# Performance work log

Hardware: AMD Instinct MI355X
Metric: run time of the kernel (lower is better)

Reference implementation:

```python
import jax, jax.numpy as jnp
import numpy as np

N_NODES = 100000
N_EDGES = 800000
R = 3
NEG_SLOPE = 0.2


def gat_conv(x, src, dst, W, al, ar, b, n_nodes):
    """One DGL-style GATConv for a single relation.
    x: [N, F_in], W: [F_in, H, D], al/ar/b: [H, D]. Returns [N, H, D]."""
    h = jnp.einsum('nf,fhd->nhd', x, W)          # [N, H, D]
    el = (h * al).sum(-1)                         # [N, H]
    er = (h * ar).sum(-1)                         # [N, H]
    e = jax.nn.leaky_relu(el[src] + er[dst], NEG_SLOPE)   # [E, H]
    # segment softmax over destination nodes
    m = jax.ops.segment_max(e, dst, num_segments=n_nodes)  # [N, H]
    ex = jnp.exp(e - m[dst])                                # [E, H]
    denom = jax.ops.segment_sum(ex, dst, num_segments=n_nodes)  # [N, H]
    alpha = ex / denom[dst]                                 # [E, H]
    msg = alpha[:, :, None] * h[src]                        # [E, H, D]
    out = jax.ops.segment_sum(msg, dst, num_segments=n_nodes)   # [N, H, D]
    return out + b


def setup_inputs() -> dict:
    key = jax.random.key(0)
    ks = jax.random.split(key, 12)
    d = {
        'x': jax.random.normal(ks[0], (N_NODES, 128), dtype=jnp.float32),
        'src': jax.random.randint(ks[1], (R, N_EDGES), 0, N_NODES, dtype=jnp.int32),
        'dst': jax.random.randint(ks[2], (R, N_EDGES), 0, N_NODES, dtype=jnp.int32),
        'W1': jax.random.normal(ks[3], (R, 128, 2, 64), dtype=jnp.float32) * 0.1,
        'al1': jax.random.normal(ks[4], (R, 2, 64), dtype=jnp.float32) * 0.1,
        'ar1': jax.random.normal(ks[5], (R, 2, 64), dtype=jnp.float32) * 0.1,
        'b1': jax.random.normal(ks[6], (R, 2, 64), dtype=jnp.float32) * 0.1,
        'W2': jax.random.normal(ks[7], (R, 128, 2, 64), dtype=jnp.float32) * 0.1,
        'al2': jax.random.normal(ks[8], (R, 2, 64), dtype=jnp.float32) * 0.1,
        'ar2': jax.random.normal(ks[9], (R, 2, 64), dtype=jnp.float32) * 0.1,
        'b2': jax.random.normal(ks[10], (R, 2, 64), dtype=jnp.float32) * 0.1,
    }
    return d


def reference(x, src, dst, W1, al1, ar1, b1, W2, al2, ar2, b2):
    n = x.shape[0]
    # layer 1: sum over relations (HeteroGraphConv aggregate='sum')
    h1 = sum(gat_conv(x, src[r], dst[r], W1[r], al1[r], ar1[r], b1[r], n)
             for r in range(R))                   # [N, 2, 64]
    h1 = jax.nn.relu(h1).reshape(n, -1)           # flatten heads -> [N, 128]
    # layer 2
    h2 = sum(gat_conv(h1, src[r], dst[r], W2[r], al2[r], ar2[r], b2[r], n)
             for r in range(R))                   # [N, 2, 64]
    return h2.mean(axis=1)                        # [N, 64]
```

## Files before the change

kernel.cpp:

```cpp
#include <hip/hip_runtime.h>
#include <hip/hip_bf16.h>
#include <math.h>

#define NF 128
#define NBKT 256
#define BCAP 11264
#define SPANCAP 2048

typedef __attribute__((ext_vector_type(8))) short short8v;
typedef __attribute__((ext_vector_type(4))) float float4v;

__device__ inline float leaky02(float v) { return v >= 0.0f ? v : 0.2f * v; }

__device__ inline unsigned short f2bf(float x) {
    unsigned u = __float_as_uint(x);
    u = u + 0x7fffu + ((u >> 16) & 1u);
    return (unsigned short)(u >> 16);
}
__device__ inline float bf2f(unsigned short h) {
    return __uint_as_float(((unsigned)h) << 16);
}

__device__ inline int rl_i(int v, int lane) {
    return __builtin_amdgcn_readlane(v, lane);
}
__device__ inline float rl_f(float v, int lane) {
    return __uint_as_float(__builtin_amdgcn_readlane(__float_as_uint(v), lane));
}

__global__ __launch_bounds__(256) void prep(
    const float* __restrict__ W1, const float* __restrict__ W2,
    const float* __restrict__ al1, const float* __restrict__ ar1,
    const float* __restrict__ b1,
    const float* __restrict__ al2, const float* __restrict__ ar2,
    const float* __restrict__ b2,
    unsigned short* __restrict__ WThi, unsigned short* __restrict__ WTlo,
    float* __restrict__ P, float* __restrict__ bs)
{
    int i = blockIdx.x * 256 + threadIdx.x;
    if (i < 6 * 16384) {
        int m = i >> 14, rem = i & 16383, k = rem >> 7, col = rem & 127;
        const float* Wm = (m < 3) ? W1 + (size_t)m * 16384
                                  : W2 + (size_t)(m - 3) * 16384;
        float v = Wm[k * 128 + col];
        unsigned short h = f2bf(v);
        WThi[(size_t)m * 16384 + col * 128 + k] = h;
        WTlo[(size_t)m * 16384 + col * 128 + k] = f2bf(v - bf2f(h));
    } else if (i < 6 * 16384 + 3072) {
        int idx = i - 6 * 16384;
        int m = idx >> 9, rem = idx & 511, f = rem >> 2, c = rem & 3;
        int head = c & 1;
        const float* Wm = (m < 3) ? W1 + (size_t)m * 16384
                                  : W2 + (size_t)(m - 3) * 16384;
        const float* vec;
        if (m < 3) vec = ((c < 2) ? al1 : ar1) + m * 128 + head * 64;
        else       vec = ((c < 2) ? al2 : ar2) + (m - 3) * 128 + head * 64;
        float s = 0.f;
        for (int d = 0; d < 64; d++) s += Wm[f * 128 + head * 64 + d] * vec[d];
        P[m * 512 + f * 4 + c] = s;
    } else if (i < 6 * 16384 + 3072 + 256) {
        int idx = i - 6 * 16384 - 3072;
        int layer = idx >> 7, cc = idx & 127;
        const float* b = layer ? b2 : b1;
        bs[layer * 128 + cc] = b[cc] + b[128 + cc] + b[256 + cc];
    }
}

__global__ __launch_bounds__(256) void bucket_count(
    const int* __restrict__ dst, int* __restrict__ bcnt,
    int E, int N, int span)
{
    __shared__ int h[NBKT];
    h[threadIdx.x] = 0;
    __syncthreads();
    const int tot = 3 * E;
    for (int e = blockIdx.x * 256 + threadIdx.x; e < tot; e += gridDim.x * 256) {
        int r = (e >= 2 * E) ? 2 : (e >= E ? 1 : 0);
        int key = r * N + dst[e];
        atomicAdd(&h[key / span], 1);
    }
    __syncthreads();
    atomicAdd(&bcnt[threadIdx.x], h[threadIdx.x]);
}

__global__ __launch_bounds__(256) void scan256(
    const int* __restrict__ bcnt, int* __restrict__ bktbase,
    int* __restrict__ gtail, int* __restrict__ rowptr, int n3)
{
    __shared__ int s[256];
    int t = threadIdx.x;
    int v = bcnt[t];
    s[t] = v;
    __syncthreads();
    for (int off = 1; off < 256; off <<= 1) {
        int x = (t >= off) ? s[t - off] : 0;
        __syncthreads();
        s[t] += x;
        __syncthreads();
    }
    int excl = s[t] - v;
    bktbase[t] = excl;
    gtail[t] = excl;
    if (t == 255) { bktbase[256] = s[255]; rowptr[n3] = s[255]; }
}

__global__ __launch_bounds__(256) void partition(
    const int* __restrict__ src, const int* __restrict__ dst,
    int* __restrict__ gtail, int2* __restrict__ pairs,
    int E, int N, int span)
{
    __shared__ int cnts[NBKT];
    __shared__ int gbase[NBKT];
    const int tot = 3 * E;
    const int per = (tot + gridDim.x - 1) / gridDim.x;
    const int e0 = blockIdx.x * per;
    const int e1 = min(tot, e0 + per);

    for (int tile = e0; tile < e1; tile += 2048) {
        int tend = min(e1, tile + 2048);
        cnts[threadIdx.x] = 0;
        __syncthreads();
        int myb[8], myoff[8], mykey[8], mysrc[8];
        int cnt_i = 0;
        for (int e = tile + threadIdx.x; e < tend; e += 256) {
            int r = (e >= 2 * E) ? 2 : (e >= E ? 1 : 0);
            int key = r * N + dst[e];
            int b = key / span;
            myb[cnt_i] = b; mykey[cnt_i] = key; mysrc[cnt_i] = src[e];
            myoff[cnt_i] = atomicAdd(&cnts[b], 1);
            cnt_i++;
        }
        __syncthreads();
        gbase[threadIdx.x] = atomicAdd(&gtail[threadIdx.x], cnts[threadIdx.x]);
        __syncthreads();
        for (int i = 0; i < cnt_i; i++)
            pairs[gbase[myb[i]] + myoff[i]] = make_int2(mykey[i], mysrc[i]);
        __syncthreads();
    }
}

__global__ __launch_bounds__(256) void place_build(
    const int2* __restrict__ pairs, const int* __restrict__ bktbase,
    int* __restrict__ rowptr, int* __restrict__ csr_src,
    int n3, int span)
{
    __shared__ int lbase[SPANCAP];
    __shared__ int acnt[SPANCAP];
    __shared__ int csr_l[BCAP];
    __shared__ int stot[256];

    const int b = blockIdx.x;
    const int t = threadIdx.x;
    const int klo = b * span;
    const int khi = min(n3, klo + span);
    const int kcount = khi - klo;
    if (kcount <= 0) return;
    const int p0 = bktbase[b], p1 = bktbase[b + 1];
    const int count = p1 - p0;

    for (int k = t; k < kcount; k += 256) lbase[k] = 0;
    __syncthreads();
    for (int i = t; i < count; i += 256)
        atomicAdd(&lbase[pairs[p0 + i].x - klo], 1);
    __syncthreads();

    const int kpt = (kcount + 255) / 256;
    const int my0 = t * kpt;
    int myn = kcount - my0;
    myn = myn < 0 ? 0 : (myn > kpt ? kpt : myn);
    int vals[8];
    int sum = 0;
    for (int i = 0; i < myn; i++) { vals[i] = lbase[my0 + i]; sum += vals[i]; }
    stot[t] = sum;
    __syncthreads();
    for (int off = 1; off < 256; off <<= 1) {
        int x = (t >= off) ? stot[t - off] : 0;
        __syncthreads();
        stot[t] += x;
        __syncthreads();
    }
    int run = stot[t] - sum;
    for (int i = 0; i < myn; i++) {
        lbase[my0 + i] = run;
        rowptr[klo + my0 + i] = p0 + run;
        run += vals[i];
    }
    for (int k = t; k < kcount; k += 256) acnt[k] = 0;
    __syncthreads();

    if (count <= BCAP) {
        for (int i = t; i < count; i += 256) {
            int2 kv = pairs[p0 + i];
            int k = kv.x - klo;
            int pos = lbase[k] + atomicAdd(&acnt[k], 1);
            csr_l[pos] = kv.y;
        }
        __syncthreads();
        for (int i = t; i < count; i += 256)
            csr_src[p0 + i] = csr_l[i];
    } else {
        for (int i = t; i < count; i += 256) {
            int2 kv = pairs[p0 + i];
            int k = kv.x - klo;
            int pos = p0 + lbase[k] + atomicAdd(&acnt[k], 1);
            csr_src[pos] = kv.y;
        }
    }
}

__global__ __launch_bounds__(256) void elproj(
    const float* __restrict__ Xin, const float* __restrict__ P,
    float* __restrict__ elr, unsigned short* __restrict__ Xb, int n)
{
    __shared__ float Xs[16][128];
    __shared__ float Ps[1536];
    int t = threadIdx.x;
    int n0 = blockIdx.x * 16;

    for (int i = t; i < 1536; i += 256) Ps[i] = P[i];
    {
        int row = t >> 4, cb = (t & 15) * 8;
        int gn = n0 + row;
        float4 a = make_float4(0, 0, 0, 0), b = make_float4(0, 0, 0, 0);
        if (gn < n) {
            a = *(const float4*)(Xin + (size_t)gn * 128 + cb);
            b = *(const float4*)(Xin + (size_t)gn * 128 + cb + 4);
        }
        *(float4*)&Xs[row][cb]     = a;
        *(float4*)&Xs[row][cb + 4] = b;
    }
    __syncthreads();

    if (t < 192) {
        int nl = t / 12, c = t % 12, r = c >> 2, j = c & 3;
        int gn = n0 + nl;
        if (gn < n) {
            float sum = 0.f;
            for (int k = 0; k < 128; k++)
                sum += Xs[nl][k] * Ps[r * 512 + k * 4 + j];
            elr[(size_t)gn * 12 + c] = sum;
        }
    }
    {
        int row = t >> 4, db = (t & 15) * 4;
        int gn = n0 + row;
        if (gn < n) {
#pragma unroll
            for (int i2 = 0; i2 < 4; i2++) {
                int d = db + i2;
                ushort2 v;
                v.x = f2bf(Xs[row][d]);
                v.y = f2bf(Xs[row][64 + d]);
                *(ushort2*)(Xb + (size_t)gn * 128 + 2 * d) = v;
            }
        }
    }
}

__global__ __launch_bounds__(256) void aggregate3(
    const int* __restrict__ rowptr, const int* __restrict__ csr_src,
    const float* __restrict__ elr, const unsigned short* __restrict__ Xb,
    unsigned short* __restrict__ Xag0, unsigned short* __restrict__ Xag1,
    unsigned short* __restrict__ Xag2, int n)
{
    int node = (int)((blockIdx.x * 256 + threadIdx.x) >> 6);
    int lane = threadIdx.x & 63;
    if (node >= n) return;

    int beg0 = rowptr[node],         end0 = rowptr[node + 1];
    int beg1 = rowptr[n + node],     end1 = rowptr[n + node + 1];
    int beg2 = rowptr[2 * n + node], end2 = rowptr[2 * n + node + 1];
    int deg0 = end0 - beg0, deg1 = end1 - beg1, deg2 = end2 - beg2;

    const float* erp = elr + (size_t)node * 12;
    float er00 = erp[2],  er01 = erp[3];
    float er10 = erp[6],  er11 = erp[7];
    float er20 = erp[10], er21 = erp[11];

    float a000 = 0.f, a001 = 0.f, a010 = 0.f, a011 = 0.f;
    float a100 = 0.f, a101 = 0.f, a110 = 0.f, a111 = 0.f;
    float a200 = 0.f, a201 = 0.f, a210 = 0.f, a211 = 0.f;

    if (deg0 <= 64 && deg1 <= 64 && deg2 <= 64) {
        int s0 = 0, s1 = 0, s2 = 0;
        if (lane < deg0) s0 = csr_src[beg0 + lane];
        if (lane < deg1) s1 = csr_src[beg1 + lane];
        if (lane < deg2) s2 = csr_src[beg2 + lane];
        float v00 = -INFINITY, v01 = -INFINITY;
        float v10 = -INFINITY, v11 = -INFINITY;
        float v20 = -INFINITY, v21 = -INFINITY;
        if (lane < deg0) {
            float2 e = *(const float2*)(elr + (size_t)s0 * 12);
            v00 = leaky02(e.x + er00); v01 = leaky02(e.y + er01);
        }
        if (lane < deg1) {
            float2 e = *(const float2*)(elr + (size_t)s1 * 12 + 4);
            v10 = leaky02(e.x + er10); v11 = leaky02(e.y + er11);
        }
        if (lane < deg2) {
            float2 e = *(const float2*)(elr + (size_t)s2 * 12 + 8);
            v20 = leaky02(e.x + er20); v21 = leaky02(e.y + er21);
        }
        float M00 = v00, M01 = v01, M10 = v10, M11 = v11, M20 = v20, M21 = v21;
#pragma unroll
        for (int off = 32; off; off >>= 1) {
            M00 = fmaxf(M00, __shfl_xor(M00, off, 64));
            M01 = fmaxf(M01, __shfl_xor(M01, off, 64));
            M10 = fmaxf(M10, __shfl_xor(M10, off, 64));
            M11 = fmaxf(M11, __shfl_xor(M11, off, 64));
            M20 = fmaxf(M20, __shfl_xor(M20, off, 64));
            M21 = fmaxf(M21, __shfl_xor(M21, off, 64));
        }
        float x00 = (lane < deg0) ? __expf(v00 - M00) : 0.f;
        float x01 = (lane < deg0) ? __expf(v01 - M01) : 0.f;
        float x10 = (lane < deg1) ? __expf(v10 - M10) : 0.f;
        float x11 = (lane < deg1) ? __expf(v11 - M11) : 0.f;
        float x20 = (lane < deg2) ? __expf(v20 - M20) : 0.f;
        float x21 = (lane < deg2) ? __expf(v21 - M21) : 0.f;
        float S00 = x00, S01 = x01, S10 = x10, S11 = x11, S20 = x20, S21 = x21;
#pragma unroll
        for (int off = 32; off; off >>= 1) {
            S00 += __shfl_xor(S00, off, 64);
            S01 += __shfl_xor(S01, off, 64);
            S10 += __shfl_xor(S10, off, 64);
            S11 += __shfl_xor(S11, off, 64);
            S20 += __shfl_xor(S20, off, 64);
            S21 += __shfl_xor(S21, off, 64);
        }
        float w00 = x00 / S00, w01 = x01 / S01;
        float w10 = x10 / S10, w11 = x11 / S11;
        float w20 = x20 / S20, w21 = x21 / S21;

        const char* XbB = (const char*)Xb;
        const unsigned int voff = 4u * (unsigned)lane;
        int dmax = max(deg0, max(deg1, deg2));
        for (int j0 = 0; j0 < dmax; j0 += 4) {
            unsigned int g0[4], g1[4], g2[4];
            float p00[4], p01[4], p10[4], p11[4], p20[4], p21[4];
#pragma unroll
            for (int j = 0; j < 4; j++) {
                int e = j0 + j;
                if (e < deg0) {
                    int ss = rl_i(s0, e);
                    p00[j] = rl_f(w00, e);
                    p01[j] = rl_f(w01, e);
                    g0[j] = *(const unsigned int*)(XbB + (size_t)ss * 256 + voff);
                }
                if (e < deg1) {
                    int ss = rl_i(s1, e);
                    p10[j] = rl_f(w10, e);
                    p11[j] = rl_f(w11, e);
                    g1[j] = *(const unsigned int*)(XbB + (size_t)ss * 256 + voff);
                }
                if (e < deg2) {
                    int ss = rl_i(s2, e);
                    p20[j] = rl_f(w20, e);
                    p21[j] = rl_f(w21, e);
                    g2[j] = *(const unsigned int*)(XbB + (size_t)ss * 256 + voff);
                }
            }
#pragma unroll
            for (int j = 0; j < 4; j++) {
                int e = j0 + j;
                if (e < deg0) {
                    float xa = __uint_as_float(g0[j] << 16);
                    float xb = __uint_as_float(g0[j] & 0xffff0000u);
                    a000 = fmaf(p00[j], xa, a000); a001 = fmaf(p00[j], xb, a001);
                    a010 = fmaf(p01[j], xa, a010); a011 = fmaf(p01[j], xb, a011);
                }
                if (e < deg1) {
                    float xa = __uint_as_float(g1[j] << 16);
                    float xb = __uint_as_float(g1[j] & 0xffff0000u);
                    a100 = fmaf(p10[j], xa, a100); a101 = fmaf(p10[j], xb, a101);
                    a110 = fmaf(p11[j], xa, a110); a111 = fmaf(p11[j], xb, a111);
                }
                if (e < deg2) {
                    float xa = __uint_as_float(g2[j] << 16);
                    float xb = __uint_as_float(g2[j] & 0xffff0000u);
                    a200 = fmaf(p20[j], xa, a200); a201 = fmaf(p20[j], xb, a201);
                    a210 = fmaf(p21[j], xa, a210); a211 = fmaf(p21[j], xb, a211);
                }
            }
        }
    } else {
#pragma unroll
        for (int r = 0; r < 3; r++) {
            int beg = (r == 0) ? beg0 : (r == 1) ? beg1 : beg2;
            int end = (r == 0) ? end0 : (r == 1) ? end1 : end2;
            if (beg >= end) continue;
            int roff = r * 4;
            float er0 = (r == 0) ? er00 : (r == 1) ? er10 : er20;
            float er1 = (r == 0) ? er01 : (r == 1) ? er11 : er21;
            float m0 = -INFINITY, m1 = -INFINITY, d0 = 0.f, d1 = 0.f;
            for (int c0 = beg; c0 < end; c0 += 64) {
                int i = c0 + lane;
                float v0 = -INFINITY, v1 = -INFINITY;
                if (i < end) {
                    int s = csr_src[i];
                    float2 e = *(const float2*)(elr + (size_t)s * 12 + roff);
                    v0 = leaky02(e.x + er0);
                    v1 = leaky02(e.y + er1);
                }
                float M0 = v0, M1 = v1;
#pragma unroll
                for (int off = 32; off; off >>= 1) {
                    M0 = fmaxf(M0, __shfl_xor(M0, off, 64));
                    M1 = fmaxf(M1, __shfl_xor(M1, off, 64));
                }
                float x0 = (i < end) ? __expf(v0 - M0) : 0.f;
                float x1 = (i < end) ? __expf(v1 - M1) : 0.f;
                float S0 = x0, S1 = x1;
#pragma unroll
                for (int off = 32; off; off >>= 1) {
                    S0 += __shfl_xor(S0, off, 64);
                    S1 += __shfl_xor(S1, off, 64);
                }
                float nm0 = fmaxf(m0, M0), nm1 = fmaxf(m1, M1);
                d0 = d0 * __expf(m0 - nm0) + S0 * __expf(M0 - nm0);
                d1 = d1 * __expf(m1 - nm1) + S1 * __expf(M1 - nm1);
                m0 = nm0; m1 = nm1;
            }
            float inv0 = 1.f / d0, inv1 = 1.f / d1;
            float b00 = 0.f, b01 = 0.f, b10 = 0.f, b11 = 0.f;
            for (int c0 = beg; c0 < end; c0 += 64) {
                int i = c0 + lane;
                int cn = min(64, end - c0);
                int s = 0; float w0 = 0.f, w1 = 0.f;
                if (i < end) {
                    s = csr_src[i];
                    float2 e = *(const float2*)(elr + (size_t)s * 12 + roff);
                    w0 = __expf(leaky02(e.x + er0) - m0) * inv0;
                    w1 = __expf(leaky02(e.y + er1) - m1) * inv1;
                }
                for (int j = 0; j < cn; j++) {
                    int ss    = __shfl(s, j, 64);
                    float ww0 = __shfl(w0, j, 64);
                    float ww1 = __shfl(w1, j, 64);
                    ushort2 xv = *(const ushort2*)(Xb + (size_t)ss * 128 + 2 * lane);
                    float xa = bf2f(xv.x), xb = bf2f(xv.y);
                    b00 += ww0 * xa; b01 += ww0 * xb;
                    b10 += ww1 * xa; b11 += ww1 * xb;
                }
            }
            if (r == 0) { a000 = b00; a001 = b01; a010 = b10; a011 = b11; }
            else if (r == 1) { a100 = b00; a101 = b01; a110 = b10; a111 = b11; }
            else { a200 = b00; a201 = b01; a210 = b10; a211 = b11; }
        }
    }

    unsigned short* x0 = Xag0 + (size_t)node * 256;
    x0[lane]       = f2bf(a000);
    x0[64 + lane]  = f2bf(a001);
    x0[128 + lane] = f2bf(a010);
    x0[192 + lane] = f2bf(a011);
    unsigned short* x1 = Xag1 + (size_t)node * 256;
    x1[lane]       = f2bf(a100);
    x1[64 + lane]  = f2bf(a101);
    x1[128 + lane] = f2bf(a110);
    x1[192 + lane] = f2bf(a111);
    unsigned short* x2 = Xag2 + (size_t)node * 256;
    x2[lane]       = f2bf(a200);
    x2[64 + lane]  = f2bf(a201);
    x2[128 + lane] = f2bf(a210);
    x2[192 + lane] = f2bf(a211);
}

__global__ __launch_bounds__(512) void gemm3(
    const unsigned short* __restrict__ Xag0,
    const unsigned short* __restrict__ Xag1,
    const unsigned short* __restrict__ Xag2,
    const unsigned short* __restrict__ WThi, const unsigned short* __restrict__ WTlo,
    const float* __restrict__ bs,
    const float* __restrict__ Pn,
    float* __restrict__ elrO, unsigned short* __restrict__ XbO,
    float* __restrict__ out,
    int n, int layer2)
{
    __shared__ short Wl[2 * 16384];
    __shared__ float Ps[1536];
    __shared__ float bsS[128];
    const int t    = threadIdx.x;
    const int row0 = blockIdx.x * 128;

    if (!layer2) for (int i = t; i < 1536; i += 512) Ps[i] = Pn[i];
    if (t < 128) bsS[t] = bs[t];

    const int w  = t >> 6;
    const int l  = t & 63;
    const int lr = l & 15;
    const int lq = l >> 4;
    const int myrow = row0 + w * 16 + lr;
    const int arow  = min(myrow, n - 1);

    float4v acc[8];
#pragma unroll
    for (int g = 0; g < 8; g++) acc[g] = (float4v){0.f, 0.f, 0.f, 0.f};

#pragma unroll
    for (int r = 0; r < 3; r++) {
        const unsigned short* WhG = WThi + (size_t)r * 16384;
        const unsigned short* WlG = WTlo + (size_t)r * 16384;
        const unsigned short* Xa  = (r == 0) ? Xag0 : (r == 1) ? Xag1 : Xag2;

        __syncthreads();
        for (int i = t; i < 4096; i += 512) {
            int half = i >> 11;
            int c16  = i & 2047;
            int row  = c16 >> 4, k16 = c16 & 15;
            short8v v = *(const short8v*)((half ? WlG : WhG) + c16 * 8);
            int off = row * 256 + ((k16 * 16) ^ ((row & 7) << 4));
            *(short8v*)((char*)Wl + half * 32768 + off) = v;
        }
        __syncthreads();

        const unsigned short* xrow = Xa + (size_t)arow * 256;
        short8v a0[4], a1[4];
#pragma unroll
        for (int ks = 0; ks < 4; ks++) {
            a0[ks] = *(const short8v*)(xrow + ks * 32 + lq * 8);
            a1[ks] = *(const short8v*)(xrow + 128 + ks * 32 + lq * 8);
        }
#pragma unroll
        for (int ks = 0; ks < 4; ks++) {
#pragma unroll
            for (int g = 0; g < 8; g++) {
                int woff = (g * 16 + lr) * 256 +
                           ((ks * 64 + lq * 16) ^ ((lr & 7) << 4));
                short8v bh = *(const short8v*)((char*)Wl + woff);
                short8v bl = *(const short8v*)((char*)Wl + 32768 + woff);
                short8v xx = (g < 4) ? a0[ks] : a1[ks];
                acc[g] = __builtin_amdgcn_mfma_f32_16x16x32_bf16(xx, bh, acc[g], 0, 0, 0);
                acc[g] = __builtin_amdgcn_mfma_f32_16x16x32_bf16(xx, bl, acc[g], 0, 0, 0);
            }
        }
    }

    float bsv[8];
#pragma unroll
    for (int g = 0; g < 8; g++) bsv[g] = bsS[g * 16 + lr];

    if (!layer2) {
#pragma unroll
        for (int rr = 0; rr < 4; rr++) {
            int gr = row0 + w * 16 + lq * 4 + rr;
            if (gr >= n) continue;
            float hr[8];
#pragma unroll
            for (int g = 0; g < 8; g++)
                hr[g] = fmaxf(acc[g][rr] + bsv[g], 0.f);
            unsigned short* xo = XbO + (size_t)gr * 128;
#pragma unroll
            for (int g = 0; g < 4; g++) {
                ushort2 v; v.x = f2bf(hr[g]); v.y = f2bf(hr[g + 4]);
                *(ushort2*)(xo + 2 * (g * 16 + lr)) = v;
            }
            float ev[12];
#pragma unroll
            for (int c = 0; c < 12; c++) {
                int r3 = c >> 2, j = c & 3;
                float s = 0.f;
#pragma unroll
                for (int g = 0; g < 8; g++)
                    s += hr[g] * Ps[r3 * 512 + (g * 16 + lr) * 4 + j];
                ev[c] = s;
            }
#pragma unroll
            for (int off = 1; off < 16; off <<= 1) {
#pragma unroll
                for (int c = 0; c < 12; c++)
                    ev[c] += __shfl_xor(ev[c], off, 64);
            }
            if (lr == 0) {
                float* eo = elrO + (size_t)gr * 12;
                *(float4*)(eo)     = make_float4(ev[0], ev[1], ev[2], ev[3]);
                *(float4*)(eo + 4) = make_float4(ev[4], ev[5], ev[6], ev[7]);
                *(float4*)(eo + 8) = make_float4(ev[8], ev[9], ev[10], ev[11]);
            }
        }
    } else {
#pragma unroll
        for (int rr = 0; rr < 4; rr++) {
            int gr = row0 + w * 16 + lq * 4 + rr;
            if (gr >= n) continue;
#pragma unroll
            for (int g = 0; g < 4; g++) {
                out[(size_t)gr * 64 + g * 16 + lr] =
                    0.5f * (acc[g][rr] + acc[g + 4][rr] + bsv[g] + bsv[g + 4]);
            }
        }
    }
}

extern "C" void kernel_launch(void* const* d_in, const int* in_sizes, int n_in,
                              void* d_out, int out_size, void* d_ws, size_t ws_size,
                              hipStream_t stream)
{
    const float* x   = (const float*)d_in[0];
    const int*   src = (const int*)  d_in[1];
    const int*   dst = (const int*)  d_in[2];
    const float* W1  = (const float*)d_in[3];
    const float* al1 = (const float*)d_in[4];
    const float* ar1 = (const float*)d_in[5];
    const float* b1  = (const float*)d_in[6];
    const float* W2  = (const float*)d_in[7];
    const float* al2 = (const float*)d_in[8];
    const float* ar2 = (const float*)d_in[9];
    const float* b2  = (const float*)d_in[10];

    const int N = in_sizes[0] / NF;
    const int E = in_sizes[1] / 3;

    char* p = (char*)d_ws;
    unsigned short* Xag0 = (unsigned short*)p; p += (size_t)N * 256 * 2;
    unsigned short* Xag1 = (unsigned short*)p; p += (size_t)N * 256 * 2;
    unsigned short* Xag2 = (unsigned short*)p; p += (size_t)N * 256 * 2;
    unsigned short* XbA  = (unsigned short*)p; p += (size_t)N * 128 * 2;
    unsigned short* XbB  = (unsigned short*)p; p += (size_t)N * 128 * 2;
    float* elrA = (float*)p;                   p += (size_t)N * 12 * 4;
    float* elrB = (float*)p;                   p += (size_t)N * 12 * 4;
    unsigned short* WThi = (unsigned short*)p; p += 6 * 16384 * 2;
    unsigned short* WTlo = (unsigned short*)p; p += 6 * 16384 * 2;
    float* P  = (float*)p;                     p += 6 * 512 * 4;
    float* bs = (float*)p;                     p += 256 * 4;
    int* rowptr  = (int*)p;                    p += ((size_t)3 * N + 1) * 4;
    int* csr_src = (int*)p;                    p += (size_t)3 * E * 4;
    int* bcnt    = (int*)Xag0;
    int* bktbase = bcnt + 256;
    int* gtail   = bktbase + 288;
    int2* pairs  = (int2*)(gtail + 256);

    const int n3 = 3 * N;
    const int span = (n3 + NBKT - 1) / NBKT;

    prep<<<(6 * 16384 + 3072 + 256 + 255) / 256, 256, 0, stream>>>(
        W1, W2, al1, ar1, b1, al2, ar2, b2, WThi, WTlo, P, bs);

    hipMemsetAsync(bcnt, 0, 256 * 4, stream);
    bucket_count<<<512, 256, 0, stream>>>(dst, bcnt, E, N, span);
    scan256<<<1, 256, 0, stream>>>(bcnt, bktbase, gtail, rowptr, n3);
    partition<<<512, 256, 0, stream>>>(src, dst, gtail, pairs, E, N, span);
    place_build<<<NBKT, 256, 0, stream>>>(pairs, bktbase, rowptr, csr_src,
                                          n3, span);

    const int aggBlocks  = (N + 3) / 4;
    const int gemmBlocks = (N + 127) / 128;
    const int projBlocks = (N + 15) / 16;

    elproj<<<projBlocks, 256, 0, stream>>>(x, P, elrA, XbA, N);
    aggregate3<<<aggBlocks, 256, 0, stream>>>(
        rowptr, csr_src, elrA, XbA, Xag0, Xag1, Xag2, N);
    gemm3<<<gemmBlocks, 512, 0, stream>>>(
        Xag0, Xag1, Xag2, WThi, WTlo, bs, P + 1536,
        elrB, XbB, nullptr, N, 0);

    aggregate3<<<aggBlocks, 256, 0, stream>>>(
        rowptr, csr_src, elrB, XbB, Xag0, Xag1, Xag2, N);
    gemm3<<<gemmBlocks, 512, 0, stream>>>(
        Xag0, Xag1, Xag2, WThi + 3 * 16384, WTlo + 3 * 16384, bs + 128, nullptr,
        nullptr, nullptr, (float*)d_out, N, 1);
}
```

Measured before the change: 548.3 us.

## Aggregate with 16 lanes per node and 16-byte vector gathers

Changes aggregate3 from one 64-lane wavefront per node to 16 lanes per node, so four nodes share a wavefront. Each lane now gathers a 16-byte uint4 of bf16 features and accumulates with packed float2 math. The high-degree fallback becomes a single-pass online softmax in 16-edge chunks that rescales the accumulators. The aim is to remove idle lanes at average degree around 8 and to issue fewer, wider memory requests. In exchange it uses more registers per lane, and within a wavefront the per-edge loop runs as long as the highest-degree of its four nodes.

```diff
diff --git a/kernel.cpp b/kernel.cpp
--- a/kernel.cpp
+++ b/kernel.cpp
@@ -9,6 +9,7 @@
 
 typedef __attribute__((ext_vector_type(8))) short short8v;
 typedef __attribute__((ext_vector_type(4))) float float4v;
+typedef __attribute__((ext_vector_type(2))) float f32x2;
 
 __device__ inline float leaky02(float v) { return v >= 0.0f ? v : 0.2f * v; }
 
@@ -20,13 +21,7 @@
 __device__ inline float bf2f(unsigned short h) {
     return __uint_as_float(((unsigned)h) << 16);
 }
-
-__device__ inline int rl_i(int v, int lane) {
-    return __builtin_amdgcn_readlane(v, lane);
-}
-__device__ inline float rl_f(float v, int lane) {
-    return __uint_as_float(__builtin_amdgcn_readlane(__float_as_uint(v), lane));
-}
+__device__ inline f32x2 mk2(float s) { return (f32x2){s, s}; }
 
 __global__ __launch_bounds__(256) void prep(
     const float* __restrict__ W1, const float* __restrict__ W2,
@@ -257,14 +252,108 @@
     }
 }
 
+#define ACCUM4(gv, w0, w1, H0, H1)                                          \
+    do {                                                                    \
+        unsigned _u; f32x2 _x;                                              \
+        _u = (gv).x;                                                        \
+        _x = (f32x2){__uint_as_float(_u << 16),                             \
+                     __uint_as_float(_u & 0xffff0000u)};                    \
+        H0[0] += mk2(w0) * _x; H1[0] += mk2(w1) * _x;                       \
+        _u = (gv).y;                                                        \
+        _x = (f32x2){__uint_as_float(_u << 16),                             \
+                     __uint_as_float(_u & 0xffff0000u)};                    \
+        H0[1] += mk2(w0) * _x; H1[1] += mk2(w1) * _x;                       \
+        _u = (gv).z;                                                        \
+        _x = (f32x2){__uint_as_float(_u << 16),                             \
+                     __uint_as_float(_u & 0xffff0000u)};                    \
+        H0[2] += mk2(w0) * _x; H1[2] += mk2(w1) * _x;                       \
+        _u = (gv).w;                                                        \
+        _x = (f32x2){__uint_as_float(_u << 16),                             \
+                     __uint_as_float(_u & 0xffff0000u)};                    \
+        H0[3] += mk2(w0) * _x; H1[3] += mk2(w1) * _x;                       \
+    } while (0)
+
+__device__ inline void agg_rel_chunk(
+    int beg, int end, int l16, int gb, float er0, float er1, int roff,
+    const float* __restrict__ elr, const int* __restrict__ csr_src,
+    const char* __restrict__ XbB, int vo,
+    f32x2 (&H0)[4], f32x2 (&H1)[4])
+{
+    if (beg >= end) return;
+    float m0 = -INFINITY, m1 = -INFINITY, S0 = 0.f, S1 = 0.f;
+    for (int c0 = beg; c0 < end; c0 += 16) {
+        int i = c0 + l16;
+        int cn = min(16, end - c0);
+        int s = 0;
+        float v0 = -INFINITY, v1 = -INFINITY;
+        if (i < end) {
+            s = csr_src[i];
+            float2 e = *(const float2*)(elr + (size_t)s * 12 + roff);
+            v0 = leaky02(e.x + er0);
+            v1 = leaky02(e.y + er1);
+        }
+        float M0 = v0, M1 = v1;
+#pragma unroll
+        for (int off = 8; off; off >>= 1) {
+            M0 = fmaxf(M0, __shfl_xor(M0, off, 64));
+            M1 = fmaxf(M1, __shfl_xor(M1, off, 64));
+        }
+        float nm0 = fmaxf(m0, M0), nm1 = fmaxf(m1, M1);
+        float sc0 = __expf(m0 - nm0), sc1 = __expf(m1 - nm1);
+        float x0 = (i < end) ? __expf(v0 - nm0) : 0.f;
+        float x1 = (i < end) ? __expf(v1 - nm1) : 0.f;
+        float cS0 = x0, cS1 = x1;
+#pragma unroll
+        for (int off = 8; off; off >>= 1) {
+            cS0 += __shfl_xor(cS0, off, 64);
+            cS1 += __shfl_xor(cS1, off, 64);
+        }
+        S0 = S0 * sc0 + cS0;
+        S1 = S1 * sc1 + cS1;
+#pragma unroll
+        for (int k = 0; k < 4; k++) { H0[k] *= mk2(sc0); H1[k] *= mk2(sc1); }
+        m0 = nm0; m1 = nm1;
+        for (int j = 0; j < cn; j++) {
+            int idx = gb + j;
+            int ss   = __shfl(s, idx, 64);
+            float u0 = __shfl(x0, idx, 64);
+            float u1 = __shfl(x1, idx, 64);
+            uint4 gv = *(const uint4*)(XbB + (size_t)ss * 256 + vo);
+            ACCUM4(gv, u0, u1, H0, H1);
+        }
+    }
+    float i0 = 1.f / S0, i1 = 1.f / S1;
+#pragma unroll
+    for (int k = 0; k < 4; k++) { H0[k] *= mk2(i0); H1[k] *= mk2(i1); }
+}
+
+__device__ inline void store_agg(unsigned short* __restrict__ xr, int l16,
+                                 const f32x2 (&H0)[4], const f32x2 (&H1)[4])
+{
+    ushort4 o;
+    o.x = f2bf(H0[0][0]); o.y = f2bf(H0[1][0]);
+    o.z = f2bf(H0[2][0]); o.w = f2bf(H0[3][0]);
+    *(ushort4*)(xr + l16 * 4) = o;
+    o.x = f2bf(H0[0][1]); o.y = f2bf(H0[1][1]);
+    o.z = f2bf(H0[2][1]); o.w = f2bf(H0[3][1]);
+    *(ushort4*)(xr + 64 + l16 * 4) = o;
+    o.x = f2bf(H1[0][0]); o.y = f2bf(H1[1][0]);
+    o.z = f2bf(H1[2][0]); o.w = f2bf(H1[3][0]);
+    *(ushort4*)(xr + 128 + l16 * 4) = o;
+    o.x = f2bf(H1[0][1]); o.y = f2bf(H1[1][1]);
+    o.z = f2bf(H1[2][1]); o.w = f2bf(H1[3][1]);
+    *(ushort4*)(xr + 192 + l16 * 4) = o;
+}
+
 __global__ __launch_bounds__(256) void aggregate3(
     const int* __restrict__ rowptr, const int* __restrict__ csr_src,
     const float* __restrict__ elr, const unsigned short* __restrict__ Xb,
     unsigned short* __restrict__ Xag0, unsigned short* __restrict__ Xag1,
     unsigned short* __restrict__ Xag2, int n)
 {
-    int node = (int)((blockIdx.x * 256 + threadIdx.x) >> 6);
-    int lane = threadIdx.x & 63;
+    const int node = blockIdx.x * 16 + (threadIdx.x >> 4);
+    const int l16  = threadIdx.x & 15;
+    const int gb   = threadIdx.x & 48;
     if (node >= n) return;
 
     int beg0 = rowptr[node],         end0 = rowptr[node + 1];
@@ -273,37 +362,47 @@
     int deg0 = end0 - beg0, deg1 = end1 - beg1, deg2 = end2 - beg2;
 
     const float* erp = elr + (size_t)node * 12;
-    float er00 = erp[2],  er01 = erp[3];
-    float er10 = erp[6],  er11 = erp[7];
-    float er20 = erp[10], er21 = erp[11];
-
-    float a000 = 0.f, a001 = 0.f, a010 = 0.f, a011 = 0.f;
-    float a100 = 0.f, a101 = 0.f, a110 = 0.f, a111 = 0.f;
-    float a200 = 0.f, a201 = 0.f, a210 = 0.f, a211 = 0.f;
-
-    if (deg0 <= 64 && deg1 <= 64 && deg2 <= 64) {
+    float4 e0v = *(const float4*)(erp);
+    float4 e1v = *(const float4*)(erp + 4);
+    float4 e2v = *(const float4*)(erp + 8);
+    const float er00 = e0v.z, er01 = e0v.w;
+    const float er10 = e1v.z, er11 = e1v.w;
+    const float er20 = e2v.z, er21 = e2v.w;
+
+    f32x2 A0[4], A1[4], B0[4], B1[4], C0[4], C1[4];
+#pragma unroll
+    for (int k = 0; k < 4; k++) {
+        A0[k] = mk2(0.f); A1[k] = mk2(0.f);
+        B0[k] = mk2(0.f); B1[k] = mk2(0.f);
+        C0[k] = mk2(0.f); C1[k] = mk2(0.f);
+    }
+
+    const char* XbB = (const char*)Xb;
+    const int vo = l16 * 16;
+
+    if (deg0 <= 16 && deg1 <= 16 && deg2 <= 16) {
         int s0 = 0, s1 = 0, s2 = 0;
-        if (lane < deg0) s0 = csr_src[beg0 + lane];
-        if (lane < deg1) s1 = csr_src[beg1 + lane];
-        if (lane < deg2) s2 = csr_src[beg2 + lane];
         float v00 = -INFINITY, v01 = -INFINITY;
         float v10 = -INFINITY, v11 = -INFINITY;
         float v20 = -INFINITY, v21 = -INFINITY;
-        if (lane < deg0) {
+        if (l16 < deg0) {
+            s0 = csr_src[beg0 + l16];
             float2 e = *(const float2*)(elr + (size_t)s0 * 12);
             v00 = leaky02(e.x + er00); v01 = leaky02(e.y + er01);
         }
-        if (lane < deg1) {
+        if (l16 < deg1) {
+            s1 = csr_src[beg1 + l16];
             float2 e = *(const float2*)(elr + (size_t)s1 * 12 + 4);
             v10 = leaky02(e.x + er10); v11 = leaky02(e.y + er11);
         }
-        if (lane < deg2) {
+        if (l16 < deg2) {
+            s2 = csr_src[beg2 + l16];
             float2 e = *(const float2*)(elr + (size_t)s2 * 12 + 8);
             v20 = leaky02(e.x + er20); v21 = leaky02(e.y + er21);
         }
         float M00 = v00, M01 = v01, M10 = v10, M11 = v11, M20 = v20, M21 = v21;
 #pragma unroll
-        for (int off = 32; off; off >>= 1) {
+        for (int off = 8; off; off >>= 1) {
             M00 = fmaxf(M00, __shfl_xor(M00, off, 64));
             M01 = fmaxf(M01, __shfl_xor(M01, off, 64));
             M10 = fmaxf(M10, __shfl_xor(M10, off, 64));
@@ -311,15 +410,15 @@
             M20 = fmaxf(M20, __shfl_xor(M20, off, 64));
             M21 = fmaxf(M21, __shfl_xor(M21, off, 64));
         }
-        float x00 = (lane < deg0) ? __expf(v00 - M00) : 0.f;
-        float x01 = (lane < deg0) ? __expf(v01 - M01) : 0.f;
-        float x10 = (lane < deg1) ? __expf(v10 - M10) : 0.f;
-        float x11 = (lane < deg1) ? __expf(v11 - M11) : 0.f;
-        float x20 = (lane < deg2) ? __expf(v20 - M20) : 0.f;
-        float x21 = (lane < deg2) ? __expf(v21 - M21) : 0.f;
+        float x00 = (l16 < deg0) ? __expf(v00 - M00) : 0.f;
+        float x01 = (l16 < deg0) ? __expf(v01 - M01) : 0.f;
+        float x10 = (l16 < deg1) ? __expf(v10 - M10) : 0.f;
+        float x11 = (l16 < deg1) ? __expf(v11 - M11) : 0.f;
+        float x20 = (l16 < deg2) ? __expf(v20 - M20) : 0.f;
+        float x21 = (l16 < deg2) ? __expf(v21 - M21) : 0.f;
         float S00 = x00, S01 = x01, S10 = x10, S11 = x11, S20 = x20, S21 = x21;
 #pragma unroll
-        for (int off = 32; off; off >>= 1) {
+        for (int off = 8; off; off >>= 1) {
             S00 += __shfl_xor(S00, off, 64);
             S01 += __shfl_xor(S01, off, 64);
             S10 += __shfl_xor(S10, off, 64);
@@ -331,138 +430,43 @@
         float w10 = x10 / S10, w11 = x11 / S11;
         float w20 = x20 / S20, w21 = x21 / S21;
 
-        const char* XbB = (const char*)Xb;
-        const unsigned int voff = 4u * (unsigned)lane;
         int dmax = max(deg0, max(deg1, deg2));
-        for (int j0 = 0; j0 < dmax; j0 += 4) {
-            unsigned int g0[4], g1[4], g2[4];
-            float p00[4], p01[4], p10[4], p11[4], p20[4], p21[4];
-#pragma unroll
-            for (int j = 0; j < 4; j++) {
-                int e = j0 + j;
-                if (e < deg0) {
-                    int ss = rl_i(s0, e);
-                    p00[j] = rl_f(w00, e);
-                    p01[j] = rl_f(w01, e);
-                    g0[j] = *(const unsigned int*)(XbB + (size_t)ss * 256 + voff);
-                }
-                if (e < deg1) {
-                    int ss = rl_i(s1, e);
-                    p10[j] = rl_f(w10, e);
-                    p11[j] = rl_f(w11, e);
-                    g1[j] = *(const unsigned int*)(XbB + (size_t)ss * 256 + voff);
-                }
-                if (e < deg2) {
-                    int ss = rl_i(s2, e);
-                    p20[j] = rl_f(w20, e);
-                    p21[j] = rl_f(w21, e);
-                    g2[j] = *(const unsigned int*)(XbB + (size_t)ss * 256 + voff);
-                }
-            }
-#pragma unroll
-            for (int j = 0; j < 4; j++) {
-                int e = j0 + j;
-                if (e < deg0) {
-                    float xa = __uint_as_float(g0[j] << 16);
-                    float xb = __uint_as_float(g0[j] & 0xffff0000u);
-                    a000 = fmaf(p00[j], xa, a000); a001 = fmaf(p00[j], xb, a001);
-                    a010 = fmaf(p01[j], xa, a010); a011 = fmaf(p01[j], xb, a011);
-                }
-                if (e < deg1) {
-                    float xa = __uint_as_float(g1[j] << 16);
-                    float xb = __uint_as_float(g1[j] & 0xffff0000u);
-                    a100 = fmaf(p10[j], xa, a100); a101 = fmaf(p10[j], xb, a101);
-                    a110 = fmaf(p11[j], xa, a110); a111 = fmaf(p11[j], xb, a111);
-                }
-                if (e < deg2) {
-                    float xa = __uint_as_float(g2[j] << 16);
-                    float xb = __uint_as_float(g2[j] & 0xffff0000u);
-                    a200 = fmaf(p20[j], xa, a200); a201 = fmaf(p20[j], xb, a201);
-                    a210 = fmaf(p21[j], xa, a210); a211 = fmaf(p21[j], xb, a211);
-                }
-            }
+        for (int j = 0; j < dmax; j++) {
+            int idx = gb + j;
+            bool q0 = j < deg0, q1 = j < deg1, q2 = j < deg2;
+            uint4 g0, g1, g2;
+            float p00, p01, p10, p11, p20, p21;
+            if (q0) {
+                int ss = __shfl(s0, idx, 64);
+                p00 = __shfl(w00, idx, 64);
+                p01 = __shfl(w01, idx, 64);
+                g0 = *(const uint4*)(XbB + (size_t)ss * 256 + vo);
+            }
+            if (q1) {
+                int ss = __shfl(s1, idx, 64);
+                p10 = __shfl(w10, idx, 64);
+                p11 = __shfl(w11, idx, 64);
+                g1 = *(const uint4*)(XbB + (size_t)ss * 256 + vo);
+            }
+            if (q2) {
+                int ss = __shfl(s2, idx, 64);
+                p20 = __shfl(w20, idx, 64);
+                p21 = __shfl(w21, idx, 64);
+                g2 = *(const uint4*)(XbB + (size_t)ss * 256 + vo);
+            }
+            if (q0) ACCUM4(g0, p00, p01, A0, A1);
+            if (q1) ACCUM4(g1, p10, p11, B0, B1);
+            if (q2) ACCUM4(g2, p20, p21, C0, C1);
         }
     } else {
-#pragma unroll
-        for (int r = 0; r < 3; r++) {
-            int beg = (r == 0) ? beg0 : (r == 1) ? beg1 : beg2;
-            int end = (r == 0) ? end0 : (r == 1) ? end1 : end2;
-            if (beg >= end) continue;
-            int roff = r * 4;
-            float er0 = (r == 0) ? er00 : (r == 1) ? er10 : er20;
-            float er1 = (r == 0) ? er01 : (r == 1) ? er11 : er21;
-            float m0 = -INFINITY, m1 = -INFINITY, d0 = 0.f, d1 = 0.f;
-            for (int c0 = beg; c0 < end; c0 += 64) {
-                int i = c0 + lane;
-                float v0 = -INFINITY, v1 = -INFINITY;
-                if (i < end) {
-                    int s = csr_src[i];
-                    float2 e = *(const float2*)(elr + (size_t)s * 12 + roff);
-                    v0 = leaky02(e.x + er0);
-                    v1 = leaky02(e.y + er1);
-                }
-                float M0 = v0, M1 = v1;
-#pragma unroll
-                for (int off = 32; off; off >>= 1) {
-                    M0 = fmaxf(M0, __shfl_xor(M0, off, 64));
-                    M1 = fmaxf(M1, __shfl_xor(M1, off, 64));
-                }
-                float x0 = (i < end) ? __expf(v0 - M0) : 0.f;
-                float x1 = (i < end) ? __expf(v1 - M1) : 0.f;
-                float S0 = x0, S1 = x1;
-#pragma unroll
-                for (int off = 32; off; off >>= 1) {
-                    S0 += __shfl_xor(S0, off, 64);
-                    S1 += __shfl_xor(S1, off, 64);
-                }
-                float nm0 = fmaxf(m0, M0), nm1 = fmaxf(m1, M1);
-                d0 = d0 * __expf(m0 - nm0) + S0 * __expf(M0 - nm0);
-                d1 = d1 * __expf(m1 - nm1) + S1 * __expf(M1 - nm1);
-                m0 = nm0; m1 = nm1;
-            }
-            float inv0 = 1.f / d0, inv1 = 1.f / d1;
-            float b00 = 0.f, b01 = 0.f, b10 = 0.f, b11 = 0.f;
-            for (int c0 = beg; c0 < end; c0 += 64) {
-                int i = c0 + lane;
-                int cn = min(64, end - c0);
-                int s = 0; float w0 = 0.f, w1 = 0.f;
-                if (i < end) {
-                    s = csr_src[i];
-                    float2 e = *(const float2*)(elr + (size_t)s * 12 + roff);
-                    w0 = __expf(leaky02(e.x + er0) - m0) * inv0;
-                    w1 = __expf(leaky02(e.y + er1) - m1) * inv1;
-                }
-                for (int j = 0; j < cn; j++) {
-                    int ss    = __shfl(s, j, 64);
-                    float ww0 = __shfl(w0, j, 64);
-                    float ww1 = __shfl(w1, j, 64);
-                    ushort2 xv = *(const ushort2*)(Xb + (size_t)ss * 128 + 2 * lane);
-                    float xa = bf2f(xv.x), xb = bf2f(xv.y);
-                    b00 += ww0 * xa; b01 += ww0 * xb;
-                    b10 += ww1 * xa; b11 += ww1 * xb;
-                }
-            }
-            if (r == 0) { a000 = b00; a001 = b01; a010 = b10; a011 = b11; }
-            else if (r == 1) { a100 = b00; a101 = b01; a110 = b10; a111 = b11; }
-            else { a200 = b00; a201 = b01; a210 = b10; a211 = b11; }
-        }
-    }
-
-    unsigned short* x0 = Xag0 + (size_t)node * 256;
-    x0[lane]       = f2bf(a000);
-    x0[64 + lane]  = f2bf(a001);
-    x0[128 + lane] = f2bf(a010);
-    x0[192 + lane] = f2bf(a011);
-    unsigned short* x1 = Xag1 + (size_t)node * 256;
-    x1[lane]       = f2bf(a100);
-    x1[64 + lane]  = f2bf(a101);
-    x1[128 + lane] = f2bf(a110);
-    x1[192 + lane] = f2bf(a111);
-    unsigned short* x2 = Xag2 + (size_t)node * 256;
-    x2[lane]       = f2bf(a200);
-    x2[64 + lane]  = f2bf(a201);
-    x2[128 + lane] = f2bf(a210);
-    x2[192 + lane] = f2bf(a211);
+        agg_rel_chunk(beg0, end0, l16, gb, er00, er01, 0, elr, csr_src, XbB, vo, A0, A1);
+        agg_rel_chunk(beg1, end1, l16, gb, er10, er11, 4, elr, csr_src, XbB, vo, B0, B1);
+        agg_rel_chunk(beg2, end2, l16, gb, er20, er21, 8, elr, csr_src, XbB, vo, C0, C1);
+    }
+
+    store_agg(Xag0 + (size_t)node * 256, l16, A0, A1);
+    store_agg(Xag1 + (size_t)node * 256, l16, B0, B1);
+    store_agg(Xag2 + (size_t)node * 256, l16, C0, C1);
 }
 
 __global__ __launch_bounds__(512) void gemm3(
@@ -642,7 +646,7 @@
     place_build<<<NBKT, 256, 0, stream>>>(pairs, bktbase, rowptr, csr_src,
                                           n3, span);
 
-    const int aggBlocks  = (N + 3) / 4;
+    const int aggBlocks  = (N + 15) / 16;
     const int gemmBlocks = (N + 127) / 128;
     const int projBlocks = (N + 15) / 16;
 
```

Measured after the change: 577.1 us. 1.05x slower.
